# Performance work log

Hardware: AMD Instinct MI355X
Metric: run time of the kernel (lower is better)

## Reference

```python
import jax, jax.numpy as jnp
import numpy as np

C_S, C_HID, H, P, V = 128, 16, 12, 4, 8
EPS = 1e-08
SOFTPLUS_INV_1 = 0.541324854612918


def _pts_from_linear(x, n_pts):
    # torch: split [..., 3*n] into 3 chunks of n, stack on dim=-1 -> [..., n, 3]
    B, N = x.shape[:2]
    return jnp.moveaxis(x.reshape(B, N, 3, n_pts), -2, -1)


def setup_inputs() -> dict:
    key = jax.random.key(0)
    ks = jax.random.split(key, 16)
    B, N = 2, 512
    hc = H * C_HID            # 192
    hpq = H * P * 3           # 144
    hpkv = H * (P + V) * 3    # 432
    cat_dim = H * (C_HID + V * 4)  # 576
    sc = 0.02
    inp = {
        "s": jax.random.normal(ks[0], (B, N, C_S), jnp.float32),
        "R": jax.random.normal(ks[1], (B, N, 3, 3), jnp.float32),
        "t": jax.random.normal(ks[2], (B, N, 3), jnp.float32),
        "pair_mask": jnp.ones((B, N, N), jnp.float32),
        "Wq": jax.random.normal(ks[3], (C_S, hc), jnp.float32) * sc,
        "bq": jnp.zeros((hc,), jnp.float32),
        "Wkv": jax.random.normal(ks[4], (C_S, 2 * hc), jnp.float32) * sc,
        "bkv": jnp.zeros((2 * hc,), jnp.float32),
        "Wqp": jax.random.normal(ks[5], (C_S, hpq), jnp.float32) * sc,
        "bqp": jnp.zeros((hpq,), jnp.float32),
        "Wkvp": jax.random.normal(ks[6], (C_S, hpkv), jnp.float32) * sc,
        "bkvp": jnp.zeros((hpkv,), jnp.float32),
        "head_weights": jnp.full((H,), SOFTPLUS_INV_1, jnp.float32),
        "Wout": jax.random.normal(ks[7], (cat_dim, C_S), jnp.float32) * sc,
        "bout": jnp.zeros((C_S,), jnp.float32),
    }
    return inp


def reference(s, R, t, pair_mask, Wq, bq, Wkv, bkv, Wqp, bqp, Wkvp, bkvp,
              head_weights, Wout, bout):
    B, N, _ = s.shape
    # scalar q/k/v
    q = (s @ Wq + bq).reshape(B, N, H, C_HID)
    kv = (s @ Wkv + bkv).reshape(B, N, H, 2 * C_HID)
    k, v = kv[..., :C_HID], kv[..., C_HID:]

    # point q/k/v in global frame: R x + t
    qp = _pts_from_linear(s @ Wqp + bqp, H * P)           # [B,N,HP,3]
    qp = jnp.einsum('bnij,bnpj->bnpi', R, qp) + t[:, :, None]
    qp = qp.reshape(B, N, H, P, 3)
    kvp = _pts_from_linear(s @ Wkvp + bkvp, H * (P + V))  # [B,N,H(P+V),3]
    kvp = jnp.einsum('bnij,bnpj->bnpi', R, kvp) + t[:, :, None]
    kvp = kvp.reshape(B, N, H, P + V, 3)
    kp, vp = kvp[..., :P, :], kvp[..., P:, :]

    # scalar attention logits [B,H,N,N]
    a = jnp.einsum('bihc,bjhc->bhij', q, k) * (1.0 / np.sqrt(3 * C_HID))

    # point-distance bias: sum_p ||q_i - k_j||^2 via |q|^2+|k|^2-2q.k
    sq_q = jnp.sum(qp * qp, axis=(-1, -2))   # [B,N,H]
    sq_k = jnp.sum(kp * kp, axis=(-1, -2))   # [B,N,H]
    cross = jnp.einsum('bihpc,bjhpc->bhij', qp, kp)
    d2 = (jnp.swapaxes(sq_q, 1, 2)[..., :, None]
          + jnp.swapaxes(sq_k, 1, 2)[..., None, :]
          - 2.0 * cross)                      # [B,H,N,N]
    hw = jax.nn.softplus(head_weights) * np.sqrt(1.0 / (3 * (P * 9.0 / 2)))
    pt_att = d2 * hw[None, :, None, None] * (-0.5)

    square_mask = 100000.0 * (pair_mask - 1.0)            # [B,N,N]
    a = jax.nn.softmax(a + pt_att + square_mask[:, None], axis=-1)

    # scalar output
    o = jnp.einsum('bhij,bjhc->bihc', a, v).reshape(B, N, H * C_HID)

    # point output, rotated back to local frame: R^T (x - t) form -> R^T x - t
    o_pt = jnp.einsum('bhij,bjhvc->bihvc', a, vp)         # [B,N,H,V,3]
    o_pt = jnp.einsum('bnji,bnhvj->bnhvi', R, o_pt) - t[:, :, None, None]
    o_pt_norm = jnp.sqrt(jnp.sum(o_pt * o_pt, axis=-1) + EPS).reshape(B, N, H * V)
    o_pt_flat = o_pt.reshape(B, N, H * V, 3)

    cat = jnp.concatenate(
        [o, o_pt_flat[..., 0], o_pt_flat[..., 1], o_pt_flat[..., 2], o_pt_norm],
        axis=-1)                                           # [B,N,576]
    return cat @ Wout + bout
```

## Files before the change

### kernel.cpp

```cpp
#include <hip/hip_runtime.h>
#include <hip/hip_bf16.h>
#include <math.h>

#define H_    12
#define B_    2
#define N_    512
#define BH_   (B_*H_)
#define QSCALE 0.14433756729740643f
#define CPT_K  0.13608276348795434f

#define OFF_RAW  0
#define OFF_APK  1179648
#define OFF_WPP  1245184
#define OFF_WOP  1318912
#define OFF_BIA  1355776
#define OFF_QB   1356928
#define OFF_KP   1553536
#define OFF_VP   1750144
#define OFF_SA   2045056
#define OFF_SB   2057344
#define OFF_CATP 2069632

typedef __attribute__((ext_vector_type(8))) short sh8;
typedef __attribute__((ext_vector_type(4))) float f32x4;
typedef unsigned short u16t;

static __device__ __forceinline__ u16t f2b(float x) {
    __hip_bfloat16 h = __float2bfloat16(x);
    return *reinterpret_cast<u16t*>(&h);
}
static __device__ __forceinline__ int catp_idx(int tok, int col) {
    return (tok >> 4)*9216 + (col >> 5)*512 + ((col >> 3) & 3)*128
         + (tok & 15)*8 + (col & 7);
}

__global__ __launch_bounds__(256) void convert_kernel(
    const float* __restrict__ s,
    const float* __restrict__ Wq,  const float* __restrict__ bq,
    const float* __restrict__ Wkv, const float* __restrict__ bkv,
    const float* __restrict__ Wqp, const float* __restrict__ bqp,
    const float* __restrict__ Wkvp,const float* __restrict__ bkvp,
    const float* __restrict__ Wout, float* __restrict__ ws)
{
    const int g = blockIdx.x * 256 + threadIdx.x;
    union { sh8 v; u16t u[8]; } pk;

    if (g < 16384) {
        int u = g;
        int m = u & 63, kq = (u >> 6) & 3, ks = (u >> 8) & 3, mt = u >> 10;
        int tok = mt*64 + m, k0 = ks*32 + kq*8;
        const float* src = s + tok*128 + k0;
        #pragma unroll
        for (int j = 0; j < 8; ++j) pk.u[j] = f2b(src[j]);
        *((sh8*)((u16t*)(ws + OFF_APK)) + u) = pk.v;
    } else if (g < 34816) {
        int u = g - 16384;
        int n = u & 63, kq = (u >> 6) & 3, ks = (u >> 8) & 3, nt = u >> 10;
        int col = nt*64 + n, k0 = ks*32 + kq*8;
        const float* w; int lc, od;
        if (col < 192)      { w = Wq;   lc = col;     od = 192; }
        else if (col < 576) { w = Wkv;  lc = col-192; od = 384; }
        else if (col < 720) { w = Wqp;  lc = col-576; od = 144; }
        else                { w = Wkvp; lc = col-720; od = 432; }
        #pragma unroll
        for (int j = 0; j < 8; ++j) pk.u[j] = f2b(w[(k0+j)*od + lc]);
        *((sh8*)((u16t*)(ws + OFF_WPP)) + u) = pk.v;
    } else if (g < 44032) {
        int u = g - 34816;
        int n = u & 63, kq = (u >> 6) & 3, rem = u >> 8;
        int ks = rem % 18, nt = rem / 18;
        int col = nt*64 + n, k0 = ks*32 + kq*8;
        #pragma unroll
        for (int j = 0; j < 8; ++j) pk.u[j] = f2b(Wout[(k0+j)*128 + col]);
        *((sh8*)((u16t*)(ws + OFF_WOP)) + u) = pk.v;
    } else if (g < 45184) {
        int col = g - 44032;
        float bv;
        if (col < 192)      bv = bq[col];
        else if (col < 576) bv = bkv[col-192];
        else if (col < 720) bv = bqp[col-576];
        else                bv = bkvp[col-720];
        ws[OFF_BIA + col] = bv;
    }
}

__global__ __launch_bounds__(256) void gemm_proj(float* __restrict__ ws)
{
    const int tid = threadIdx.x;
    const int w = tid >> 6, lane = tid & 63;
    const int lx = lane & 15, kq = lane >> 4;
    const int nt = blockIdx.x, mt = blockIdx.y;

    const sh8* Ap = (const sh8*)((const u16t*)(ws + OFF_APK));
    const sh8* Bp = (const sh8*)((const u16t*)(ws + OFF_WPP));

    f32x4 acc[4];
    #pragma unroll
    for (int nq = 0; nq < 4; ++nq) acc[nq] = (f32x4){0.f,0.f,0.f,0.f};

    #pragma unroll
    for (int ks = 0; ks < 4; ++ks) {
        sh8 af = Ap[((mt*4 + ks)*4 + kq)*64 + w*16 + lx];
        #pragma unroll
        for (int nq = 0; nq < 4; ++nq) {
            sh8 bf = Bp[((nt*4 + ks)*4 + kq)*64 + nq*16 + lx];
            acc[nq] = __builtin_amdgcn_mfma_f32_16x16x32_bf16(af, bf, acc[nq], 0, 0, 0);
        }
    }
    float* raw = ws + OFF_RAW;
    const float* bias = ws + OFF_BIA;
    #pragma unroll
    for (int nq = 0; nq < 4; ++nq) {
        int col = nt*64 + nq*16 + lx;
        float bv = bias[col];
        #pragma unroll
        for (int r = 0; r < 4; ++r) {
            int tok = mt*64 + w*16 + kq*4 + r;
            raw[tok*1152 + col] = acc[nq][r] + bv;
        }
    }
}

__global__ __launch_bounds__(256) void pack_kernel(
    const float* __restrict__ Rg, const float* __restrict__ tg,
    const float* __restrict__ hwg, float* __restrict__ ws)
{
    __shared__ float ldsP[4][1152];
    __shared__ float rotQ[4][48][3];
    __shared__ float rotK[4][48][3];
    __shared__ float rotV[4][96][3];

    const float* raw = ws + OFF_RAW;
    u16t* Qb = (u16t*)(ws + OFF_QB);
    u16t* Kp = (u16t*)(ws + OFF_KP);
    u16t* Vp = (u16t*)(ws + OFF_VP);
    float* sa_g = ws + OFF_SA;
    float* sb_g = ws + OFF_SB;

    const int tid  = threadIdx.x;
    const int tok0 = blockIdx.x * 4;
    const int b    = tok0 >> 9, n0 = tok0 & 511;

    for (int idx = tid; idx < 1152; idx += 256) {
        int tk = idx / 288, c4 = idx % 288;
        *(float4*)&ldsP[tk][c4*4] = *(const float4*)(raw + (tok0+tk)*1152 + c4*4);
    }
    __syncthreads();

    for (int idx = tid; idx < 4*48; idx += 256) {
        int tk = idx / 48, p = idx % 48;
        int tok = tok0 + tk;
        const float* Rr = Rg + tok*9;
        const float* tr = tg + tok*3;
        float x0 = ldsP[tk][576 +   0 + p];
        float x1 = ldsP[tk][576 +  48 + p];
        float x2 = ldsP[tk][576 +  96 + p];
        rotQ[tk][p][0] = Rr[0]*x0 + Rr[1]*x1 + Rr[2]*x2 + tr[0];
        rotQ[tk][p][1] = Rr[3]*x0 + Rr[4]*x1 + Rr[5]*x2 + tr[1];
        rotQ[tk][p][2] = Rr[6]*x0 + Rr[7]*x1 + Rr[8]*x2 + tr[2];
    }
    for (int idx = tid; idx < 4*144; idx += 256) {
        int tk = idx / 144, p = idx % 144;
        int tok = tok0 + tk;
        const float* Rr = Rg + tok*9;
        const float* tr = tg + tok*3;
        float x0 = ldsP[tk][720 +   0 + p];
        float x1 = ldsP[tk][720 + 144 + p];
        float x2 = ldsP[tk][720 + 288 + p];
        float r0 = Rr[0]*x0 + Rr[1]*x1 + Rr[2]*x2 + tr[0];
        float r1 = Rr[3]*x0 + Rr[4]*x1 + Rr[5]*x2 + tr[1];
        float r2 = Rr[6]*x0 + Rr[7]*x1 + Rr[8]*x2 + tr[2];
        int h = p / 12, pp = p % 12;
        if (pp < 4) {
            rotK[tk][h*4+pp][0] = r0; rotK[tk][h*4+pp][1] = r1; rotK[tk][h*4+pp][2] = r2;
        } else {
            rotV[tk][h*8+pp-4][0] = r0; rotV[tk][h*8+pp-4][1] = r1; rotV[tk][h*8+pp-4][2] = r2;
        }
    }
    __syncthreads();

    for (int idx = tid; idx < 96; idx += 256) {
        int tk = idx / 24, r2 = idx % 24, h = r2 >> 1, half = r2 & 1;
        float hx = hwg[h];
        float sp = (hx > 20.f) ? hx : log1pf(__expf(hx));
        float c_pt = -0.5f * sp * CPT_K;
        union { sh8 v[2]; u16t u[16]; } pk;
        if (half == 0) {
            #pragma unroll
            for (int e = 0; e < 16; ++e) pk.u[e] = f2b(ldsP[tk][h*16 + e] * QSCALE);
        } else {
            float qs = -2.f * c_pt;
            #pragma unroll
            for (int e = 0; e < 12; ++e) pk.u[e] = f2b(rotQ[tk][h*4 + e/3][e%3] * qs);
            pk.u[12]=0; pk.u[13]=0; pk.u[14]=0; pk.u[15]=0;
        }
        u16t* dst = Qb + ((b*H_+h)*N_ + n0 + tk)*32 + half*16;
        *(sh8*)dst = pk.v[0];
        *(sh8*)(dst+8) = pk.v[1];
    }
    for (int idx = tid; idx < 192; idx += 256) {
        int tk = idx / 48, r2 = idx % 48, h = r2 >> 2, kq = r2 & 3;
        int j = n0 + tk, bh = b*H_ + h;
        union { sh8 v; u16t u[8]; } pk;
        #pragma unroll
        for (int e = 0; e < 8; ++e) {
            int c = kq*8 + e;
            float val;
            if (c < 16)      val = ldsP[tk][192 + h*32 + c];
            else if (c < 28) val = rotK[tk][h*4 + (c-16)/3][(c-16)%3];
            else             val = 0.f;
            pk.u[e] = f2b(val);
        }
        *(sh8*)(Kp + bh*16384 + (j>>4)*512 + kq*128 + (j&15)*8) = pk.v;
    }
    for (int idx = tid; idx < 480; idx += 256) {
        int h = idx / 40, d = idx % 40;
        int bh = b*H_ + h;
        #pragma unroll
        for (int tk = 0; tk < 4; ++tk) {
            int j = n0 + tk;
            float val;
            if (d < 16) val = ldsP[tk][192 + h*32 + 16 + d];
            else        val = rotV[tk][h*8 + (d-16)/3][(d-16)%3];
            Vp[bh*24576 + (j>>5)*1536 + (d>>4)*512 + ((j>>3)&3)*128
               + (d&15)*8 + (j&7)] = f2b(val);
        }
    }
    for (int idx = tid; idx < 48; idx += 256) {
        int tk = idx / 12, h = idx % 12;
        float hx = hwg[h];
        float sp = (hx > 20.f) ? hx : log1pf(__expf(hx));
        float c_pt = -0.5f * sp * CPT_K;
        float sq = 0.f, sk = 0.f;
        #pragma unroll
        for (int pp = 0; pp < 4; ++pp)
            #pragma unroll
            for (int c = 0; c < 3; ++c) {
                float a = rotQ[tk][h*4+pp][c]; sq += a*a;
                float k = rotK[tk][h*4+pp][c]; sk += k*k;
            }
        sa_g[(b*H_+h)*N_ + n0 + tk] = c_pt * sq;
        sb_g[(b*H_+h)*N_ + n0 + tk] = c_pt * sk;
    }
}

__global__ __launch_bounds__(256) void attn_kernel(
    const float* __restrict__ Rg, const float* __restrict__ tg,
    const float* __restrict__ maskg, float* __restrict__ ws)
{
    __shared__ u16t smP[4*16*72];
    __shared__ float obuf[4*16*32];

    const u16t* Qb = (const u16t*)(ws + OFF_QB);
    const u16t* Kp = (const u16t*)(ws + OFF_KP);
    const u16t* Vp = (const u16t*)(ws + OFF_VP);
    const float* sa_g = ws + OFF_SA;
    const float* sb_g = ws + OFF_SB;
    u16t* catp = (u16t*)(ws + OFF_CATP);

    const int tid  = threadIdx.x;
    const int w    = tid >> 6, lane = tid & 63;
    const int kq   = lane >> 4, lx = lane & 15;
    const int bh   = blockIdx.x >> 3;
    const int it   = blockIdx.x & 7;
    const int b    = bh / H_, h = bh % H_;
    const int i0   = it * 64;

    sh8 qfrag = *(const sh8*)(Qb + (bh*N_ + i0 + w*16 + lx)*32 + kq*8);
    float sa_r[4];
    #pragma unroll
    for (int r = 0; r < 4; ++r)
        sa_r[r] = sa_g[bh*N_ + i0 + w*16 + kq*4 + r];

    float m_run[4] = {-1e30f,-1e30f,-1e30f,-1e30f};
    float l_run[4] = {0.f,0.f,0.f,0.f};
    f32x4 oc0 = {0.f,0.f,0.f,0.f}, oc1 = oc0, oc2 = oc0;

    const float* mrow = maskg + (size_t)(b*N_ + i0 + w*16 + kq*4)*N_ + lx;
    u16t* pw = smP + w*1152;

    for (int jt = 0; jt < 8; ++jt) {
        const int j0 = jt * 64;

        f32x4 sc[4];
        #pragma unroll
        for (int st = 0; st < 4; ++st) {
            sh8 kf = *(const sh8*)(Kp + bh*16384 + (jt*4+st)*512 + kq*128 + lx*8);
            f32x4 z = {0.f,0.f,0.f,0.f};
            sc[st] = __builtin_amdgcn_mfma_f32_16x16x32_bf16(qfrag, kf, z, 0, 0, 0);
        }
        float sbv[4];
        #pragma unroll
        for (int st = 0; st < 4; ++st) sbv[st] = sb_g[bh*N_ + j0 + st*16 + lx];
        float mb[16];
        #pragma unroll
        for (int r = 0; r < 4; ++r)
            #pragma unroll
            for (int st = 0; st < 4; ++st)
                mb[r*4+st] = mrow[r*N_ + j0 + st*16];

        float L[16];
        #pragma unroll
        for (int st = 0; st < 4; ++st)
            #pragma unroll
            for (int r = 0; r < 4; ++r)
                L[st*4+r] = sc[st][r] + sa_r[r] + sbv[st] + 1e5f*(mb[r*4+st] - 1.f);

        #pragma unroll
        for (int r = 0; r < 4; ++r) {
            float tm = fmaxf(fmaxf(L[0*4+r], L[1*4+r]), fmaxf(L[2*4+r], L[3*4+r]));
            tm = fmaxf(tm, __shfl_xor(tm, 1));
            tm = fmaxf(tm, __shfl_xor(tm, 2));
            tm = fmaxf(tm, __shfl_xor(tm, 4));
            tm = fmaxf(tm, __shfl_xor(tm, 8));
            float mnew = fmaxf(m_run[r], tm);
            float al = __expf(m_run[r] - mnew);
            m_run[r] = mnew;
            l_run[r] *= al;
            oc0[r] *= al; oc1[r] *= al; oc2[r] *= al;
        }
        #pragma unroll
        for (int st = 0; st < 4; ++st)
            #pragma unroll
            for (int r = 0; r < 4; ++r) {
                float p = __expf(L[st*4+r] - m_run[r]);
                l_run[r] += p;
                pw[(kq*4+r)*72 + st*16 + lx] = f2b(p);
            }
        #pragma unroll
        for (int c = 0; c < 2; ++c) {
            sh8 pa = *(const sh8*)(pw + lx*72 + c*32 + kq*8);
            #pragma unroll
            for (int nq = 0; nq < 3; ++nq) {
                sh8 vf = *(const sh8*)(Vp + bh*24576 + (jt*2+c)*1536 + nq*512
                                        + kq*128 + lx*8);
                if (nq == 0) oc0 = __builtin_amdgcn_mfma_f32_16x16x32_bf16(pa, vf, oc0, 0,0,0);
                if (nq == 1) oc1 = __builtin_amdgcn_mfma_f32_16x16x32_bf16(pa, vf, oc1, 0,0,0);
                if (nq == 2) oc2 = __builtin_amdgcn_mfma_f32_16x16x32_bf16(pa, vf, oc2, 0,0,0);
            }
        }
    }

    float linv[4];
    #pragma unroll
    for (int r = 0; r < 4; ++r) {
        float l = l_run[r];
        l += __shfl_xor(l, 1); l += __shfl_xor(l, 2);
        l += __shfl_xor(l, 4); l += __shfl_xor(l, 8);
        linv[r] = 1.f / l;
    }

    #pragma unroll
    for (int r = 0; r < 4; ++r) {
        int tok = b*N_ + i0 + w*16 + kq*4 + r;
        catp[catp_idx(tok, h*16 + lx)] = f2b(oc0[r] * linv[r]);
        obuf[(w*16 + kq*4 + r)*32 + lx]      = oc1[r] * linv[r];
        obuf[(w*16 + kq*4 + r)*32 + 16 + lx] = oc2[r] * linv[r];
    }
    __syncthreads();

    #pragma unroll
    for (int tsk = 0; tsk < 2; ++tsk) {
        int task = lane + tsk*64;
        int r = task >> 3, pv = task & 7;
        int tok = b*N_ + i0 + w*16 + r;
        const float* Rr = Rg + tok*9;
        const float* tr = tg + tok*3;
        float g0 = obuf[(w*16 + r)*32 + pv*3 + 0];
        float g1 = obuf[(w*16 + r)*32 + pv*3 + 1];
        float g2 = obuf[(w*16 + r)*32 + pv*3 + 2];
        float px = Rr[0]*g0 + Rr[3]*g1 + Rr[6]*g2 - tr[0];
        float py = Rr[1]*g0 + Rr[4]*g1 + Rr[7]*g2 - tr[1];
        float pz = Rr[2]*g0 + Rr[5]*g1 + Rr[8]*g2 - tr[2];
        float nrm = sqrtf(px*px + py*py + pz*pz + 1e-8f);
        catp[catp_idx(tok, 192 + h*8 + pv)] = f2b(px);
        catp[catp_idx(tok, 288 + h*8 + pv)] = f2b(py);
        catp[catp_idx(tok, 384 + h*8 + pv)] = f2b(pz);
        catp[catp_idx(tok, 480 + h*8 + pv)] = f2b(nrm);
    }
}

__global__ __launch_bounds__(256) void out_kernel(
    const float* __restrict__ bout, const float* __restrict__ ws,
    float* __restrict__ out)
{
    const int tid = threadIdx.x;
    const int w = tid >> 6, lane = tid & 63;
    const int lx = lane & 15, kq = lane >> 4;
    const int nt = blockIdx.x, mt = blockIdx.y;

    const sh8* Ap = (const sh8*)((const u16t*)(ws + OFF_CATP));
    const sh8* Bp = (const sh8*)((const u16t*)(ws + OFF_WOP));

    f32x4 acc = {0.f,0.f,0.f,0.f};
    for (int ks = 0; ks < 18; ++ks) {
        sh8 af = Ap[((mt*18 + ks)*4 + kq)*16 + lx];
        sh8 bf = Bp[((nt*18 + ks)*4 + kq)*64 + w*16 + lx];
        acc = __builtin_amdgcn_mfma_f32_16x16x32_bf16(af, bf, acc, 0, 0, 0);
    }
    int col = nt*64 + w*16 + lx;
    float bv = bout[col];
    #pragma unroll
    for (int r = 0; r < 4; ++r) {
        int row = mt*16 + kq*4 + r;
        out[row*128 + col] = acc[r] + bv;
    }
}

extern "C" void kernel_launch(void* const* d_in, const int* in_sizes, int n_in,
                              void* d_out, int out_size, void* d_ws, size_t ws_size,
                              hipStream_t stream) {
    const float* s    = (const float*)d_in[0];
    const float* R    = (const float*)d_in[1];
    const float* t    = (const float*)d_in[2];
    const float* mask = (const float*)d_in[3];
    const float* Wq   = (const float*)d_in[4];
    const float* bq   = (const float*)d_in[5];
    const float* Wkv  = (const float*)d_in[6];
    const float* bkv  = (const float*)d_in[7];
    const float* Wqp  = (const float*)d_in[8];
    const float* bqp  = (const float*)d_in[9];
    const float* Wkvp = (const float*)d_in[10];
    const float* bkvp = (const float*)d_in[11];
    const float* hw   = (const float*)d_in[12];
    const float* Wout = (const float*)d_in[13];
    const float* bout = (const float*)d_in[14];
    float* ws  = (float*)d_ws;
    float* out = (float*)d_out;

    convert_kernel<<<177, 256, 0, stream>>>(s, Wq, bq, Wkv, bkv,
                                            Wqp, bqp, Wkvp, bkvp, Wout, ws);
    gemm_proj<<<dim3(18, 16), 256, 0, stream>>>(ws);
    pack_kernel<<<B_*N_/4, 256, 0, stream>>>(R, t, hw, ws);
    attn_kernel<<<BH_*8, 256, 0, stream>>>(R, t, mask, ws);
    out_kernel<<<dim3(2, 64), 256, 0, stream>>>(bout, ws, out);
}
```

Measured before the change: 114.0 us.

## Fuse projection GEMM into pack kernel and split attention KV range across waves

```diff
diff --git a/kernel.cpp b/kernel.cpp
--- a/kernel.cpp
+++ b/kernel.cpp
@@ -9,8 +9,6 @@
 #define QSCALE 0.14433756729740643f
 #define CPT_K  0.13608276348795434f
 
-#define OFF_RAW  0
-#define OFF_APK  1179648
 #define OFF_WPP  1245184
 #define OFF_WOP  1318912
 #define OFF_BIA  1355776
@@ -35,7 +33,6 @@
 }
 
 __global__ __launch_bounds__(256) void convert_kernel(
-    const float* __restrict__ s,
     const float* __restrict__ Wq,  const float* __restrict__ bq,
     const float* __restrict__ Wkv, const float* __restrict__ bkv,
     const float* __restrict__ Wqp, const float* __restrict__ bqp,
@@ -45,16 +42,8 @@
     const int g = blockIdx.x * 256 + threadIdx.x;
     union { sh8 v; u16t u[8]; } pk;
 
-    if (g < 16384) {
+    if (g < 18432) {
         int u = g;
-        int m = u & 63, kq = (u >> 6) & 3, ks = (u >> 8) & 3, mt = u >> 10;
-        int tok = mt*64 + m, k0 = ks*32 + kq*8;
-        const float* src = s + tok*128 + k0;
-        #pragma unroll
-        for (int j = 0; j < 8; ++j) pk.u[j] = f2b(src[j]);
-        *((sh8*)((u16t*)(ws + OFF_APK)) + u) = pk.v;
-    } else if (g < 34816) {
-        int u = g - 16384;
         int n = u & 63, kq = (u >> 6) & 3, ks = (u >> 8) & 3, nt = u >> 10;
         int col = nt*64 + n, k0 = ks*32 + kq*8;
         const float* w; int lc, od;
@@ -65,16 +54,16 @@
         #pragma unroll
         for (int j = 0; j < 8; ++j) pk.u[j] = f2b(w[(k0+j)*od + lc]);
         *((sh8*)((u16t*)(ws + OFF_WPP)) + u) = pk.v;
-    } else if (g < 44032) {
-        int u = g - 34816;
+    } else if (g < 27648) {
+        int u = g - 18432;
         int n = u & 63, kq = (u >> 6) & 3, rem = u >> 8;
         int ks = rem % 18, nt = rem / 18;
         int col = nt*64 + n, k0 = ks*32 + kq*8;
         #pragma unroll
         for (int j = 0; j < 8; ++j) pk.u[j] = f2b(Wout[(k0+j)*128 + col]);
         *((sh8*)((u16t*)(ws + OFF_WOP)) + u) = pk.v;
-    } else if (g < 45184) {
-        int col = g - 44032;
+    } else if (g < 28800) {
+        int col = g - 27648;
         float bv;
         if (col < 192)      bv = bq[col];
         else if (col < 576) bv = bkv[col-192];
@@ -84,53 +73,13 @@
     }
 }
 
-__global__ __launch_bounds__(256) void gemm_proj(float* __restrict__ ws)
-{
-    const int tid = threadIdx.x;
-    const int w = tid >> 6, lane = tid & 63;
-    const int lx = lane & 15, kq = lane >> 4;
-    const int nt = blockIdx.x, mt = blockIdx.y;
-
-    const sh8* Ap = (const sh8*)((const u16t*)(ws + OFF_APK));
-    const sh8* Bp = (const sh8*)((const u16t*)(ws + OFF_WPP));
-
-    f32x4 acc[4];
-    #pragma unroll
-    for (int nq = 0; nq < 4; ++nq) acc[nq] = (f32x4){0.f,0.f,0.f,0.f};
-
-    #pragma unroll
-    for (int ks = 0; ks < 4; ++ks) {
-        sh8 af = Ap[((mt*4 + ks)*4 + kq)*64 + w*16 + lx];
-        #pragma unroll
-        for (int nq = 0; nq < 4; ++nq) {
-            sh8 bf = Bp[((nt*4 + ks)*4 + kq)*64 + nq*16 + lx];
-            acc[nq] = __builtin_amdgcn_mfma_f32_16x16x32_bf16(af, bf, acc[nq], 0, 0, 0);
-        }
-    }
-    float* raw = ws + OFF_RAW;
-    const float* bias = ws + OFF_BIA;
-    #pragma unroll
-    for (int nq = 0; nq < 4; ++nq) {
-        int col = nt*64 + nq*16 + lx;
-        float bv = bias[col];
-        #pragma unroll
-        for (int r = 0; r < 4; ++r) {
-            int tok = mt*64 + w*16 + kq*4 + r;
-            raw[tok*1152 + col] = acc[nq][r] + bv;
-        }
-    }
-}
-
-__global__ __launch_bounds__(256) void pack_kernel(
+__global__ __launch_bounds__(256) void projpack_kernel(
+    const float* __restrict__ s,
     const float* __restrict__ Rg, const float* __restrict__ tg,
     const float* __restrict__ hwg, float* __restrict__ ws)
 {
-    __shared__ float ldsP[4][1152];
-    __shared__ float rotQ[4][48][3];
-    __shared__ float rotK[4][48][3];
-    __shared__ float rotV[4][96][3];
-
-    const float* raw = ws + OFF_RAW;
+    __shared__ float ldsP[16][1160];
+
     u16t* Qb = (u16t*)(ws + OFF_QB);
     u16t* Kp = (u16t*)(ws + OFF_KP);
     u16t* Vp = (u16t*)(ws + OFF_VP);
@@ -138,28 +87,56 @@
     float* sb_g = ws + OFF_SB;
 
     const int tid  = threadIdx.x;
-    const int tok0 = blockIdx.x * 4;
+    const int w    = tid >> 6, lane = tid & 63;
+    const int kq   = lane >> 4, lx = lane & 15;
+    const int tok0 = blockIdx.x * 16;
     const int b    = tok0 >> 9, n0 = tok0 & 511;
 
-    for (int idx = tid; idx < 1152; idx += 256) {
-        int tk = idx / 288, c4 = idx % 288;
-        *(float4*)&ldsP[tk][c4*4] = *(const float4*)(raw + (tok0+tk)*1152 + c4*4);
+    sh8 afr[4];
+    #pragma unroll
+    for (int ks = 0; ks < 4; ++ks) {
+        const float* src = s + (tok0+lx)*128 + ks*32 + kq*8;
+        float4 u0 = *(const float4*)(src);
+        float4 u1 = *(const float4*)(src+4);
+        union { sh8 v; u16t u[8]; } pk;
+        pk.u[0]=f2b(u0.x); pk.u[1]=f2b(u0.y); pk.u[2]=f2b(u0.z); pk.u[3]=f2b(u0.w);
+        pk.u[4]=f2b(u1.x); pk.u[5]=f2b(u1.y); pk.u[6]=f2b(u1.z); pk.u[7]=f2b(u1.w);
+        afr[ks] = pk.v;
+    }
+
+    const sh8* Bp = (const sh8*)((const u16t*)(ws + OFF_WPP));
+    const float* bias = ws + OFF_BIA;
+
+    #pragma unroll 2
+    for (int g = 0; g < 18; ++g) {
+        int gg = w*18 + g;
+        int nt = gg >> 2, nq = gg & 3;
+        f32x4 acc = {0.f,0.f,0.f,0.f};
+        #pragma unroll
+        for (int ks = 0; ks < 4; ++ks) {
+            sh8 bf = Bp[((nt*4 + ks)*4 + kq)*64 + nq*16 + lx];
+            acc = __builtin_amdgcn_mfma_f32_16x16x32_bf16(afr[ks], bf, acc, 0, 0, 0);
+        }
+        float bv = bias[gg*16 + lx];
+        #pragma unroll
+        for (int r = 0; r < 4; ++r)
+            ldsP[kq*4 + r][gg*16 + lx] = acc[r] + bv;
     }
     __syncthreads();
 
-    for (int idx = tid; idx < 4*48; idx += 256) {
+    for (int idx = tid; idx < 16*48; idx += 256) {
         int tk = idx / 48, p = idx % 48;
         int tok = tok0 + tk;
         const float* Rr = Rg + tok*9;
         const float* tr = tg + tok*3;
-        float x0 = ldsP[tk][576 +   0 + p];
-        float x1 = ldsP[tk][576 +  48 + p];
-        float x2 = ldsP[tk][576 +  96 + p];
-        rotQ[tk][p][0] = Rr[0]*x0 + Rr[1]*x1 + Rr[2]*x2 + tr[0];
-        rotQ[tk][p][1] = Rr[3]*x0 + Rr[4]*x1 + Rr[5]*x2 + tr[1];
-        rotQ[tk][p][2] = Rr[6]*x0 + Rr[7]*x1 + Rr[8]*x2 + tr[2];
-    }
-    for (int idx = tid; idx < 4*144; idx += 256) {
+        float x0 = ldsP[tk][576 +  0 + p];
+        float x1 = ldsP[tk][576 + 48 + p];
+        float x2 = ldsP[tk][576 + 96 + p];
+        ldsP[tk][576 +  0 + p] = Rr[0]*x0 + Rr[1]*x1 + Rr[2]*x2 + tr[0];
+        ldsP[tk][576 + 48 + p] = Rr[3]*x0 + Rr[4]*x1 + Rr[5]*x2 + tr[1];
+        ldsP[tk][576 + 96 + p] = Rr[6]*x0 + Rr[7]*x1 + Rr[8]*x2 + tr[2];
+    }
+    for (int idx = tid; idx < 16*144; idx += 256) {
         int tk = idx / 144, p = idx % 144;
         int tok = tok0 + tk;
         const float* Rr = Rg + tok*9;
@@ -167,19 +144,13 @@
         float x0 = ldsP[tk][720 +   0 + p];
         float x1 = ldsP[tk][720 + 144 + p];
         float x2 = ldsP[tk][720 + 288 + p];
-        float r0 = Rr[0]*x0 + Rr[1]*x1 + Rr[2]*x2 + tr[0];
-        float r1 = Rr[3]*x0 + Rr[4]*x1 + Rr[5]*x2 + tr[1];
-        float r2 = Rr[6]*x0 + Rr[7]*x1 + Rr[8]*x2 + tr[2];
-        int h = p / 12, pp = p % 12;
-        if (pp < 4) {
-            rotK[tk][h*4+pp][0] = r0; rotK[tk][h*4+pp][1] = r1; rotK[tk][h*4+pp][2] = r2;
-        } else {
-            rotV[tk][h*8+pp-4][0] = r0; rotV[tk][h*8+pp-4][1] = r1; rotV[tk][h*8+pp-4][2] = r2;
-        }
+        ldsP[tk][720 +   0 + p] = Rr[0]*x0 + Rr[1]*x1 + Rr[2]*x2 + tr[0];
+        ldsP[tk][720 + 144 + p] = Rr[3]*x0 + Rr[4]*x1 + Rr[5]*x2 + tr[1];
+        ldsP[tk][720 + 288 + p] = Rr[6]*x0 + Rr[7]*x1 + Rr[8]*x2 + tr[2];
     }
     __syncthreads();
 
-    for (int idx = tid; idx < 96; idx += 256) {
+    for (int idx = tid; idx < 16*24; idx += 256) {
         int tk = idx / 24, r2 = idx % 24, h = r2 >> 1, half = r2 & 1;
         float hx = hwg[h];
         float sp = (hx > 20.f) ? hx : log1pf(__expf(hx));
@@ -191,42 +162,46 @@
         } else {
             float qs = -2.f * c_pt;
             #pragma unroll
-            for (int e = 0; e < 12; ++e) pk.u[e] = f2b(rotQ[tk][h*4 + e/3][e%3] * qs);
+            for (int e = 0; e < 12; ++e)
+                pk.u[e] = f2b(ldsP[tk][576 + (e%3)*48 + h*4 + e/3] * qs);
             pk.u[12]=0; pk.u[13]=0; pk.u[14]=0; pk.u[15]=0;
         }
         u16t* dst = Qb + ((b*H_+h)*N_ + n0 + tk)*32 + half*16;
         *(sh8*)dst = pk.v[0];
         *(sh8*)(dst+8) = pk.v[1];
     }
-    for (int idx = tid; idx < 192; idx += 256) {
-        int tk = idx / 48, r2 = idx % 48, h = r2 >> 2, kq = r2 & 3;
+    for (int idx = tid; idx < 16*48; idx += 256) {
+        int tk = idx / 48, r2 = idx % 48, h = r2 >> 2, fq = r2 & 3;
         int j = n0 + tk, bh = b*H_ + h;
         union { sh8 v; u16t u[8]; } pk;
         #pragma unroll
         for (int e = 0; e < 8; ++e) {
-            int c = kq*8 + e;
+            int c = fq*8 + e;
             float val;
             if (c < 16)      val = ldsP[tk][192 + h*32 + c];
-            else if (c < 28) val = rotK[tk][h*4 + (c-16)/3][(c-16)%3];
+            else if (c < 28) val = ldsP[tk][720 + ((c-16)%3)*144 + h*12 + (c-16)/3];
             else             val = 0.f;
             pk.u[e] = f2b(val);
         }
-        *(sh8*)(Kp + bh*16384 + (j>>4)*512 + kq*128 + (j&15)*8) = pk.v;
-    }
-    for (int idx = tid; idx < 480; idx += 256) {
-        int h = idx / 40, d = idx % 40;
+        *(sh8*)(Kp + bh*16384 + (j>>4)*512 + fq*128 + (j&15)*8) = pk.v;
+    }
+    for (int idx = tid; idx < 960; idx += 256) {
+        int h = idx / 80, r2 = idx % 80, d = r2 >> 1, grp = r2 & 1;
         int bh = b*H_ + h;
-        #pragma unroll
-        for (int tk = 0; tk < 4; ++tk) {
-            int j = n0 + tk;
+        union { sh8 v; u16t u[8]; } pk;
+        #pragma unroll
+        for (int e = 0; e < 8; ++e) {
+            int tk = grp*8 + e;
             float val;
             if (d < 16) val = ldsP[tk][192 + h*32 + 16 + d];
-            else        val = rotV[tk][h*8 + (d-16)/3][(d-16)%3];
-            Vp[bh*24576 + (j>>5)*1536 + (d>>4)*512 + ((j>>3)&3)*128
-               + (d&15)*8 + (j&7)] = f2b(val);
-        }
-    }
-    for (int idx = tid; idx < 48; idx += 256) {
+            else        val = ldsP[tk][720 + ((d-16)%3)*144 + h*12 + 4 + (d-16)/3];
+            pk.u[e] = f2b(val);
+        }
+        int j = n0 + grp*8;
+        *(sh8*)(Vp + bh*24576 + (j>>5)*1536 + (d>>4)*512 + ((j>>3)&3)*128
+                + (d&15)*8) = pk.v;
+    }
+    for (int idx = tid; idx < 16*12; idx += 256) {
         int tk = idx / 12, h = idx % 12;
         float hx = hwg[h];
         float sp = (hx > 20.f) ? hx : log1pf(__expf(hx));
@@ -236,20 +211,21 @@
         for (int pp = 0; pp < 4; ++pp)
             #pragma unroll
             for (int c = 0; c < 3; ++c) {
-                float a = rotQ[tk][h*4+pp][c]; sq += a*a;
-                float k = rotK[tk][h*4+pp][c]; sk += k*k;
+                float a = ldsP[tk][576 + c*48  + h*4  + pp]; sq += a*a;
+                float k = ldsP[tk][720 + c*144 + h*12 + pp]; sk += k*k;
             }
         sa_g[(b*H_+h)*N_ + n0 + tk] = c_pt * sq;
         sb_g[(b*H_+h)*N_ + n0 + tk] = c_pt * sk;
     }
 }
 
-__global__ __launch_bounds__(256) void attn_kernel(
+__global__ __launch_bounds__(512, 2) void attn_kernel(
     const float* __restrict__ Rg, const float* __restrict__ tg,
     const float* __restrict__ maskg, float* __restrict__ ws)
 {
-    __shared__ u16t smP[4*16*72];
-    __shared__ float obuf[4*16*32];
+    __shared__ u16t smP[8*16*72];
+    __shared__ float mbuf[4*64*20];
+    __shared__ float obuf[64*32];
 
     const u16t* Qb = (const u16t*)(ws + OFF_QB);
     const u16t* Kp = (const u16t*)(ws + OFF_KP);
@@ -260,26 +236,28 @@
 
     const int tid  = threadIdx.x;
     const int w    = tid >> 6, lane = tid & 63;
+    const int rg   = w & 3, jh = w >> 2;
     const int kq   = lane >> 4, lx = lane & 15;
     const int bh   = blockIdx.x >> 3;
     const int it   = blockIdx.x & 7;
     const int b    = bh / H_, h = bh % H_;
     const int i0   = it * 64;
 
-    sh8 qfrag = *(const sh8*)(Qb + (bh*N_ + i0 + w*16 + lx)*32 + kq*8);
+    sh8 qfrag = *(const sh8*)(Qb + (bh*N_ + i0 + rg*16 + lx)*32 + kq*8);
     float sa_r[4];
     #pragma unroll
     for (int r = 0; r < 4; ++r)
-        sa_r[r] = sa_g[bh*N_ + i0 + w*16 + kq*4 + r];
+        sa_r[r] = sa_g[bh*N_ + i0 + rg*16 + kq*4 + r];
 
     float m_run[4] = {-1e30f,-1e30f,-1e30f,-1e30f};
     float l_run[4] = {0.f,0.f,0.f,0.f};
     f32x4 oc0 = {0.f,0.f,0.f,0.f}, oc1 = oc0, oc2 = oc0;
 
-    const float* mrow = maskg + (size_t)(b*N_ + i0 + w*16 + kq*4)*N_ + lx;
+    const float* mrow = maskg + (size_t)(b*N_ + i0 + rg*16 + kq*4)*N_ + lx;
     u16t* pw = smP + w*1152;
 
-    for (int jt = 0; jt < 8; ++jt) {
+    for (int t = 0; t < 4; ++t) {
+        const int jt = jh*4 + t;
         const int j0 = jt * 64;
 
         f32x4 sc[4];
@@ -341,42 +319,63 @@
         }
     }
 
-    float linv[4];
-    #pragma unroll
-    for (int r = 0; r < 4; ++r) {
-        float l = l_run[r];
-        l += __shfl_xor(l, 1); l += __shfl_xor(l, 2);
-        l += __shfl_xor(l, 4); l += __shfl_xor(l, 8);
-        linv[r] = 1.f / l;
-    }
-
-    #pragma unroll
-    for (int r = 0; r < 4; ++r) {
-        int tok = b*N_ + i0 + w*16 + kq*4 + r;
-        catp[catp_idx(tok, h*16 + lx)] = f2b(oc0[r] * linv[r]);
-        obuf[(w*16 + kq*4 + r)*32 + lx]      = oc1[r] * linv[r];
-        obuf[(w*16 + kq*4 + r)*32 + 16 + lx] = oc2[r] * linv[r];
+    if (jh == 1) {
+        float* mb = mbuf + (rg*64 + lane)*20;
+        #pragma unroll
+        for (int r = 0; r < 4; ++r) {
+            mb[r]      = m_run[r];
+            mb[4 + r]  = l_run[r];
+            mb[8 + r]  = oc0[r];
+            mb[12 + r] = oc1[r];
+            mb[16 + r] = oc2[r];
+        }
     }
     __syncthreads();
-
-    #pragma unroll
-    for (int tsk = 0; tsk < 2; ++tsk) {
-        int task = lane + tsk*64;
-        int r = task >> 3, pv = task & 7;
-        int tok = b*N_ + i0 + w*16 + r;
-        const float* Rr = Rg + tok*9;
-        const float* tr = tg + tok*3;
-        float g0 = obuf[(w*16 + r)*32 + pv*3 + 0];
-        float g1 = obuf[(w*16 + r)*32 + pv*3 + 1];
-        float g2 = obuf[(w*16 + r)*32 + pv*3 + 2];
-        float px = Rr[0]*g0 + Rr[3]*g1 + Rr[6]*g2 - tr[0];
-        float py = Rr[1]*g0 + Rr[4]*g1 + Rr[7]*g2 - tr[1];
-        float pz = Rr[2]*g0 + Rr[5]*g1 + Rr[8]*g2 - tr[2];
-        float nrm = sqrtf(px*px + py*py + pz*pz + 1e-8f);
-        catp[catp_idx(tok, 192 + h*8 + pv)] = f2b(px);
-        catp[catp_idx(tok, 288 + h*8 + pv)] = f2b(py);
-        catp[catp_idx(tok, 384 + h*8 + pv)] = f2b(pz);
-        catp[catp_idx(tok, 480 + h*8 + pv)] = f2b(nrm);
+    if (jh == 0) {
+        const float* mb = mbuf + (rg*64 + lane)*20;
+        float linv[4];
+        #pragma unroll
+        for (int r = 0; r < 4; ++r) {
+            float mB = mb[r];
+            float ms = fmaxf(m_run[r], mB);
+            float eA = __expf(m_run[r] - ms);
+            float eB = __expf(mB - ms);
+            float l = l_run[r]*eA + mb[4+r]*eB;
+            oc0[r] = oc0[r]*eA + mb[8+r]*eB;
+            oc1[r] = oc1[r]*eA + mb[12+r]*eB;
+            oc2[r] = oc2[r]*eA + mb[16+r]*eB;
+            l += __shfl_xor(l, 1); l += __shfl_xor(l, 2);
+            l += __shfl_xor(l, 4); l += __shfl_xor(l, 8);
+            linv[r] = 1.f / l;
+        }
+
+        #pragma unroll
+        for (int r = 0; r < 4; ++r) {
+            int tok = b*N_ + i0 + rg*16 + kq*4 + r;
+            catp[catp_idx(tok, h*16 + lx)] = f2b(oc0[r] * linv[r]);
+            obuf[(rg*16 + kq*4 + r)*32 + lx]      = oc1[r] * linv[r];
+            obuf[(rg*16 + kq*4 + r)*32 + 16 + lx] = oc2[r] * linv[r];
+        }
+
+        #pragma unroll
+        for (int tsk = 0; tsk < 2; ++tsk) {
+            int task = lane + tsk*64;
+            int r = task >> 3, pv = task & 7;
+            int tok = b*N_ + i0 + rg*16 + r;
+            const float* Rr = Rg + tok*9;
+            const float* tr = tg + tok*3;
+            float g0 = obuf[(rg*16 + r)*32 + pv*3 + 0];
+            float g1 = obuf[(rg*16 + r)*32 + pv*3 + 1];
+            float g2 = obuf[(rg*16 + r)*32 + pv*3 + 2];
+            float px = Rr[0]*g0 + Rr[3]*g1 + Rr[6]*g2 - tr[0];
+            float py = Rr[1]*g0 + Rr[4]*g1 + Rr[7]*g2 - tr[1];
+            float pz = Rr[2]*g0 + Rr[5]*g1 + Rr[8]*g2 - tr[2];
+            float nrm = sqrtf(px*px + py*py + pz*pz + 1e-8f);
+            catp[catp_idx(tok, 192 + h*8 + pv)] = f2b(px);
+            catp[catp_idx(tok, 288 + h*8 + pv)] = f2b(py);
+            catp[catp_idx(tok, 384 + h*8 + pv)] = f2b(pz);
+            catp[catp_idx(tok, 480 + h*8 + pv)] = f2b(nrm);
+        }
     }
 }
 
@@ -428,10 +427,9 @@
     float* ws  = (float*)d_ws;
     float* out = (float*)d_out;
 
-    convert_kernel<<<177, 256, 0, stream>>>(s, Wq, bq, Wkv, bkv,
+    convert_kernel<<<113, 256, 0, stream>>>(Wq, bq, Wkv, bkv,
                                             Wqp, bqp, Wkvp, bkvp, Wout, ws);
-    gemm_proj<<<dim3(18, 16), 256, 0, stream>>>(ws);
-    pack_kernel<<<B_*N_/4, 256, 0, stream>>>(R, t, hw, ws);
-    attn_kernel<<<BH_*8, 256, 0, stream>>>(R, t, mask, ws);
+    projpack_kernel<<<64, 256, 0, stream>>>(s, R, t, hw, ws);
+    attn_kernel<<<BH_*8, 512, 0, stream>>>(R, t, mask, ws);
     out_kernel<<<dim3(2, 64), 256, 0, stream>>>(bout, ws, out);
 }
```

Measured after the change: 115.1 us. Within noise of the previous version (+1.0%).
